# Performance work log

Hardware: AMD Instinct MI355X
Metric: run time of the kernel (lower is better)

Reference implementation:

```python
import jax, jax.numpy as jnp
import numpy as np
import math

B, S, D, H = 2, 2048, 1024, 16
DK = D // H


def setup_inputs() -> dict:
    key = jax.random.key(0)
    ks = jax.random.split(key, 12)
    std = 1.0 / math.sqrt(D)
    inp = {
        "query": jax.random.normal(ks[0], (B, S, D), jnp.float32),
        "key": jax.random.normal(ks[1], (B, S, D), jnp.float32),
        "value": jax.random.normal(ks[2], (B, S, D), jnp.float32),
        # causal mask, broadcast over batch and heads
        "mask": jnp.tril(jnp.ones((S, S), jnp.int32))[None, None, :, :],
        # nn.Linear weights are [out_features, in_features]
        "Wq": jax.random.uniform(ks[3], (D, D), jnp.float32, -std, std),
        "bq": jax.random.uniform(ks[4], (D,), jnp.float32, -std, std),
        "Wk": jax.random.uniform(ks[5], (D, D), jnp.float32, -std, std),
        "bk": jax.random.uniform(ks[6], (D,), jnp.float32, -std, std),
        "Wv": jax.random.uniform(ks[7], (D, D), jnp.float32, -std, std),
        "bv": jax.random.uniform(ks[8], (D,), jnp.float32, -std, std),
        "Wo": jax.random.uniform(ks[9], (D, D), jnp.float32, -std, std),
        "bo": jax.random.uniform(ks[10], (D,), jnp.float32, -std, std),
    }
    return inp


def reference(query, key, value, mask, Wq, bq, Wk, bk, Wv, bv, Wo, bo):
    q = query @ Wq.T + bq  # [B,S,D]
    k = key @ Wk.T + bk
    v = value @ Wv.T + bv
    # Faithful to the original: a raw view (reshape), NOT a head-transpose split.
    q = q.reshape(B, H, S, DK)
    k = k.reshape(B, H, S, DK)
    v = v.reshape(B, H, S, DK)
    scores = jnp.einsum("bhqd,bhkd->bhqk", q, k) / math.sqrt(DK)
    scores = jnp.where(mask == 0, jnp.float32(-1e9), scores)
    weights = jax.nn.softmax(scores, axis=-1)
    # dropout(p=0.1) is identity in eval mode
    context = jnp.einsum("bhqk,bhkd->bhqd", weights, v)
    context = context.transpose(0, 2, 1, 3).reshape(B, S, D)
    return context @ Wo.T + bo
```

## Files before the change

### kernel.cpp

```cpp
#include <hip/hip_runtime.h>
#include <hip/hip_bf16.h>

#define BB 2
#define SS 2048
#define DD 1024
#define HH 16
#define DKK 64

typedef __attribute__((ext_vector_type(4))) float  f32x4;
typedef __attribute__((ext_vector_type(8))) short  s16x8;
typedef __attribute__((ext_vector_type(4))) short  s16x4;
typedef __attribute__((ext_vector_type(4))) float  fvec4;
typedef __attribute__((ext_vector_type(2))) unsigned int u32x2;

__device__ __forceinline__ short f2bs(float f) {
    union { __hip_bfloat16 b; short s; } u;
    u.b = __float2bfloat16(f);
    return u.s;
}

__device__ __forceinline__ unsigned cvtpk(float lo, float hi) {
    unsigned r;
    asm("v_cvt_pk_bf16_f32 %0, %1, %2" : "=v"(r) : "v"(lo), "v"(hi));
    return r;
}

__device__ __forceinline__ void gload_lds16(const short* g, short* l) {
    __builtin_amdgcn_global_load_lds((const __attribute__((address_space(1))) void*)g,
                                     (__attribute__((address_space(3))) void*)l, 16, 0, 0);
}

__global__ __launch_bounds__(256) void cvt_all(
    const float* __restrict__ q,  const float* __restrict__ k,  const float* __restrict__ v,
    const float* __restrict__ wq, const float* __restrict__ wk, const float* __restrict__ wv,
    const float* __restrict__ wo,
    short* __restrict__ qo,  short* __restrict__ ko,  short* __restrict__ vo,
    short* __restrict__ wqo, short* __restrict__ wko, short* __restrict__ wvo,
    short* __restrict__ woo)
{
    const float* src; short* dst; int n;
    switch (blockIdx.y) {
        case 0: src = q;  dst = qo;  n = BB * SS * DD; break;
        case 1: src = k;  dst = ko;  n = BB * SS * DD; break;
        case 2: src = v;  dst = vo;  n = BB * SS * DD; break;
        case 3: src = wq; dst = wqo; n = DD * DD; break;
        case 4: src = wk; dst = wko; n = DD * DD; break;
        case 5: src = wv; dst = wvo; n = DD * DD; break;
        default: src = wo; dst = woo; n = DD * DD; break;
    }
    int i = (blockIdx.x * 256 + threadIdx.x) * 8;
    const int stride = gridDim.x * 256 * 8;
    for (; i < n; i += stride) {
        fvec4 a = *(const fvec4*)&src[i];
        fvec4 b = *(const fvec4*)&src[i + 4];
        s16x8 o;
        o[0] = f2bs(a[0]); o[1] = f2bs(a[1]); o[2] = f2bs(a[2]); o[3] = f2bs(a[3]);
        o[4] = f2bs(b[0]); o[5] = f2bs(b[1]); o[6] = f2bs(b[2]); o[7] = f2bs(b[3]);
        *(s16x8*)&dst[i] = o;
    }
}

template<int BN, int NXSH, bool OUTF32>
__global__ __launch_bounds__(256) void gemm_nt_v2(
    const short* __restrict__ A0, const short* __restrict__ A1, const short* __restrict__ A2,
    const short* __restrict__ B0, const short* __restrict__ B1, const short* __restrict__ B2,
    const float* __restrict__ c0, const float* __restrict__ c1, const float* __restrict__ c2,
    void* __restrict__ O0, void* __restrict__ O1, void* __restrict__ O2,
    float os0, float os1, float os2,
    int ppx, int NY, int KL, int N, int K)
{
    const int d   = blockIdx.x;
    const int xcd = d & 7;
    const int s   = d >> 3;
    const int x   = s & ((1 << NXSH) - 1);
    const int pl  = s >> NXSH;
    const int panel = xcd * ppx + pl;
    const int y   = panel % NY;
    const int z   = panel / NY;

    const short* A    = z == 0 ? A0 : (z == 1 ? A1 : A2);
    const short* Bw   = z == 0 ? B0 : (z == 1 ? B1 : B2);
    const float* bias = z == 0 ? c0 : (z == 1 ? c1 : c2);
    void* Cp          = z == 0 ? O0 : (z == 1 ? O1 : O2);
    const float oscale = z == 0 ? os0 : (z == 1 ? os1 : os2);

    __shared__ short As[128][64];
    __shared__ short Bs[BN][64];

    const int tid  = threadIdx.x;
    const int lane = tid & 63;
    const int wid  = tid >> 6;
    const int r16  = lane & 15;
    const int g    = lane >> 4;
    const int m0   = y * 128;
    const int n0   = x * BN;
    constexpr int MR = 4;
    constexpr int NR = BN / 32;
    const int wr   = (wid >> 1) * 64;
    const int wc   = (wid & 1) * (BN / 2);
    const int srow8 = lane >> 3;
    const int c8    = lane & 7;

    f32x4 acc[MR][NR];
#pragma unroll
    for (int mi = 0; mi < MR; ++mi)
#pragma unroll
        for (int ni = 0; ni < NR; ++ni) acc[mi][ni] = (f32x4){0.f, 0.f, 0.f, 0.f};

    const int csrc = (c8 ^ srow8) * 8;
    const int nk = KL >> 6;
#pragma unroll 1
    for (int kt = 0; kt < nk; ++kt) {
        const int k0 = kt * 64;
        if (kt) __syncthreads();
#pragma unroll
        for (int q = 0; q < 4; ++q) {
            const int r = wid * 32 + q * 8 + srow8;
            gload_lds16(&A[(size_t)(m0 + r) * K + k0 + csrc], &As[wid * 32 + q * 8][0]);
        }
#pragma unroll
        for (int q = 0; q < BN / 32; ++q) {
            const int r = wid * (BN / 4) + q * 8 + srow8;
            gload_lds16(&Bw[(size_t)(n0 + r) * K + k0 + csrc], &Bs[wid * (BN / 4) + q * 8][0]);
        }
        __syncthreads();

#pragma unroll
        for (int kk = 0; kk < 2; ++kk) {
            s16x8 af[MR], bf[NR];
#pragma unroll
            for (int mi = 0; mi < MR; ++mi) {
                const int row = wr + mi * 16 + r16;
                af[mi] = *(const s16x8*)&As[row][((kk * 4 + g) ^ (row & 7)) * 8];
            }
#pragma unroll
            for (int ni = 0; ni < NR; ++ni) {
                const int row = wc + ni * 16 + r16;
                bf[ni] = *(const s16x8*)&Bs[row][((kk * 4 + g) ^ (row & 7)) * 8];
            }
#pragma unroll
            for (int mi = 0; mi < MR; ++mi)
#pragma unroll
                for (int ni = 0; ni < NR; ++ni)
                    acc[mi][ni] = __builtin_amdgcn_mfma_f32_16x16x32_bf16(
                        bf[ni], af[mi], acc[mi][ni], 0, 0, 0);
        }
    }

#pragma unroll
    for (int mi = 0; mi < MR; ++mi) {
        const size_t row = (size_t)(m0 + wr + mi * 16 + r16);
#pragma unroll
        for (int ni = 0; ni < NR; ++ni) {
            const int colb = n0 + wc + ni * 16 + g * 4;
            fvec4 bv;
            if (bias) bv = *(const fvec4*)&bias[colb];
            else      bv = (fvec4){0.f, 0.f, 0.f, 0.f};
            const f32x4 a = acc[mi][ni];
            const float v0 = (a[0] + bv[0]) * oscale;
            const float v1 = (a[1] + bv[1]) * oscale;
            const float v2 = (a[2] + bv[2]) * oscale;
            const float v3 = (a[3] + bv[3]) * oscale;
            if constexpr (OUTF32) {
                fvec4 o; o[0] = v0; o[1] = v1; o[2] = v2; o[3] = v3;
                *(fvec4*)&((float*)Cp)[row * N + colb] = o;
            } else {
                u32x2 w;
                w[0] = cvtpk(v0, v1);
                w[1] = cvtpk(v2, v3);
                *(u32x2*)&((short*)Cp)[row * N + colb] = w;
            }
        }
    }
}

__global__ __launch_bounds__(256) void mha_transpose_v(
    const short* __restrict__ vp, short* __restrict__ vT)
{
    const int st = blockIdx.x;
    const int bh = blockIdx.y;
    const short* src = vp + (size_t)bh * SS * DKK;
    short*       dst = vT + (size_t)bh * SS * DKK;
    const int tid = threadIdx.x;
#pragma unroll
    for (int i = 0; i < 2; ++i) {
        const int c  = tid + i * 256;
        const int dk = c >> 3;
        const int sc = c & 7;
        const int s0 = st * 64 + sc * 8;
        s16x8 v;
#pragma unroll
        for (int j = 0; j < 8; ++j) v[j] = src[(size_t)(s0 + j) * DKK + dk];
        *(s16x8*)&dst[(size_t)dk * SS + s0] = v;
    }
}

__global__ __launch_bounds__(256, 2) void mha_attn(
    const short* __restrict__ qp, const short* __restrict__ kp,
    const short* __restrict__ vT, short* __restrict__ ctx)
{
    __shared__ short Ks[64][64];
    __shared__ short Vs[64][64];
    __shared__ short P[4][16][72];

    const int tid  = threadIdx.x;
    const int wid  = tid >> 6;
    const int lane = tid & 63;
    const int r16  = lane & 15;
    const int g    = lane >> 4;

    const int lin = blockIdx.x;
    const int xcd = lin & 7;
    const int s8  = lin >> 3;
    const int bh  = (xcd << 2) | (s8 & 3);
    const int v   = s8 >> 2;
    const int grp = (v < 16) ? v : (47 - v);
    const int b   = bh >> 4;
    const int h   = bh & 15;

    const short* Qh = qp + (size_t)bh * SS * DKK;
    const short* Kh = kp + (size_t)bh * SS * DKK;
    const short* Vh = vT + (size_t)bh * SS * DKK;

    const int srow = lane >> 3;
    const int csw  = (((lane & 7) ^ srow) & 7) * 8;
    const int r0   = wid * 16;

    const int qr0 = grp * 64 + wid * 16;
    const int nkt = grp + 1;

    const s16x8 qf0 = *(const s16x8*)&Qh[(size_t)(qr0 + r16) * DKK + g * 8];
    const s16x8 qf1 = *(const s16x8*)&Qh[(size_t)(qr0 + r16) * DKK + 32 + g * 8];

    f32x4 po[4];
#pragma unroll
    for (int i = 0; i < 4; ++i) po[i] = (f32x4){0.f, 0.f, 0.f, 0.f};
    float lsum = 0.f;

#pragma unroll 1
    for (int j = 0; j < nkt; ++j) {
        const int k0 = j * 64;
        __syncthreads();
        {
            const int rowA = r0 + srow;
            const int rowB = rowA + 8;
            gload_lds16(&Kh[(size_t)(k0 + rowA) * DKK + csw], &Ks[r0][0]);
            gload_lds16(&Kh[(size_t)(k0 + rowB) * DKK + csw], &Ks[r0 + 8][0]);
            gload_lds16(&Vh[(size_t)rowA * SS + k0 + csw], &Vs[r0][0]);
            gload_lds16(&Vh[(size_t)rowB * SS + k0 + csw], &Vs[r0 + 8][0]);
        }
        __syncthreads();

        f32x4 sc[4];
        __builtin_amdgcn_s_setprio(1);
#pragma unroll
        for (int cg = 0; cg < 4; ++cg) {
            const int R  = cg * 16 + r16;
            const int sw = R & 7;
            const s16x8 kf0 = *(const s16x8*)&Ks[R][((g ^ sw) & 7) * 8];
            const s16x8 kf1 = *(const s16x8*)&Ks[R][(((4 + g) ^ sw) & 7) * 8];
            f32x4 tt = (f32x4){0.f, 0.f, 0.f, 0.f};
            tt = __builtin_amdgcn_mfma_f32_16x16x32_bf16(kf0, qf0, tt, 0, 0, 0);
            tt = __builtin_amdgcn_mfma_f32_16x16x32_bf16(kf1, qf1, tt, 0, 0, 0);
            sc[cg] = tt;
        }
        __builtin_amdgcn_s_setprio(0);

        if (j == nkt - 1) {
#pragma unroll
            for (int cg = 0; cg < 4; ++cg)
#pragma unroll
                for (int r = 0; r < 4; ++r)
                    if (k0 + cg * 16 + g * 4 + r > qr0 + r16) sc[cg][r] = -1e9f;
        }
#pragma unroll
        for (int cg = 0; cg < 4; ++cg) {
            const float p0 = __expf(sc[cg][0]);
            const float p1 = __expf(sc[cg][1]);
            const float p2 = __expf(sc[cg][2]);
            const float p3 = __expf(sc[cg][3]);
            lsum += (p0 + p1) + (p2 + p3);
            u32x2 w;
            w[0] = cvtpk(p0, p1);
            w[1] = cvtpk(p2, p3);
            *(u32x2*)&P[wid][r16][cg * 16 + g * 4] = w;
        }
        const s16x8 pf0 = *(const s16x8*)&P[wid][r16][g * 8];
        const s16x8 pf1 = *(const s16x8*)&P[wid][r16][32 + g * 8];

        __builtin_amdgcn_s_setprio(1);
#pragma unroll
        for (int dg = 0; dg < 4; ++dg) {
            const int Rv = dg * 16 + r16;
            const int sw = Rv & 7;
            const s16x8 vf0 = *(const s16x8*)&Vs[Rv][((g ^ sw) & 7) * 8];
            const s16x8 vf1 = *(const s16x8*)&Vs[Rv][(((4 + g) ^ sw) & 7) * 8];
            po[dg] = __builtin_amdgcn_mfma_f32_16x16x32_bf16(pf0, vf0, po[dg], 0, 0, 0);
            po[dg] = __builtin_amdgcn_mfma_f32_16x16x32_bf16(pf1, vf1, po[dg], 0, 0, 0);
        }
        __builtin_amdgcn_s_setprio(0);
    }

    lsum += __shfl_xor(lsum, 16);
    lsum += __shfl_xor(lsum, 32);
    const float linv = __builtin_amdgcn_rcpf(lsum);
    float rowinv[4];
#pragma unroll
    for (int r = 0; r < 4; ++r)
        rowinv[r] = __shfl(linv, g * 4 + r);
#pragma unroll
    for (int dg = 0; dg < 4; ++dg)
#pragma unroll
        for (int r = 0; r < 4; ++r) {
            const int srw = qr0 + g * 4 + r;
            const float vv = po[dg][r] * rowinv[r];
            ctx[((size_t)(b * SS + srw)) * DD + h * 64 + dg * 16 + r16] = f2bs(vv);
        }
}

extern "C" void kernel_launch(void* const* d_in, const int* in_sizes, int n_in,
                              void* d_out, int out_size, void* d_ws, size_t ws_size,
                              hipStream_t stream) {
    const float* query = (const float*)d_in[0];
    const float* key   = (const float*)d_in[1];
    const float* value = (const float*)d_in[2];
    const float* Wq = (const float*)d_in[4];
    const float* bq = (const float*)d_in[5];
    const float* Wk = (const float*)d_in[6];
    const float* bk = (const float*)d_in[7];
    const float* Wv = (const float*)d_in[8];
    const float* bv = (const float*)d_in[9];
    const float* Wo = (const float*)d_in[10];
    const float* bo = (const float*)d_in[11];
    float* out = (float*)d_out;

    const size_t elems = (size_t)BB * SS * DD;
    const size_t wel   = (size_t)DD * DD;
    short* qx  = (short*)d_ws;
    short* kx  = qx + elems;
    short* vx  = kx + elems;
    short* wqx = vx + elems;
    short* wkx = wqx + wel;
    short* wvx = wkx + wel;
    short* wox = wvx + wel;
    short* qp  = wox + wel;
    short* kp  = qp + elems;
    short* vp  = kp + elems;
    short* vT  = qx;
    short* ctx = vx;

    cvt_all<<<dim3(1024, 7), 256, 0, stream>>>(query, key, value, Wq, Wk, Wv, Wo,
                                               qx, kx, vx, wqx, wkx, wvx, wox);
    gemm_nt_v2<128, 3, false><<<dim3(768), 256, 0, stream>>>(
        qx, kx, vx, wqx, wkx, wvx, bq, bk, bv, qp, kp, vp,
        0.125f, 1.0f, 1.0f, 12, 32, 1024, DD, DD);
    mha_transpose_v<<<dim3(SS / 64, BB * HH), 256, 0, stream>>>(vp, vT);
    mha_attn<<<dim3(1024), 256, 0, stream>>>(qp, kp, vT, ctx);
    gemm_nt_v2<64, 4, true><<<dim3(512), 256, 0, stream>>>(
        ctx, ctx, ctx, wox, wox, wox, bo, bo, bo, out, out, out,
        1.0f, 1.0f, 1.0f, 4, 32, 1024, DD, DD);
}
```

Baseline: 121.1 us.

## Use two waves per attention block, each handling 32 query rows

```diff
diff --git a/kernel.cpp b/kernel.cpp
--- a/kernel.cpp
+++ b/kernel.cpp
@@ -195,13 +195,13 @@
     }
 }
 
-__global__ __launch_bounds__(256, 2) void mha_attn(
+__global__ __launch_bounds__(128) void mha_attn(
     const short* __restrict__ qp, const short* __restrict__ kp,
     const short* __restrict__ vT, short* __restrict__ ctx)
 {
     __shared__ short Ks[64][64];
     __shared__ short Vs[64][64];
-    __shared__ short P[4][16][72];
+    __shared__ short P[2][32][72];
 
     const int tid  = threadIdx.x;
     const int wid  = tid >> 6;
@@ -224,34 +224,40 @@
 
     const int srow = lane >> 3;
     const int csw  = (((lane & 7) ^ srow) & 7) * 8;
-    const int r0   = wid * 16;
-
-    const int qr0 = grp * 64 + wid * 16;
+
+    const int qr0 = grp * 64 + wid * 32;
     const int nkt = grp + 1;
 
-    const s16x8 qf0 = *(const s16x8*)&Qh[(size_t)(qr0 + r16) * DKK + g * 8];
-    const s16x8 qf1 = *(const s16x8*)&Qh[(size_t)(qr0 + r16) * DKK + 32 + g * 8];
-
-    f32x4 po[4];
-#pragma unroll
-    for (int i = 0; i < 4; ++i) po[i] = (f32x4){0.f, 0.f, 0.f, 0.f};
-    float lsum = 0.f;
+    s16x8 qf[2][2];
+#pragma unroll
+    for (int hh = 0; hh < 2; ++hh)
+#pragma unroll
+        for (int sl = 0; sl < 2; ++sl)
+            qf[hh][sl] = *(const s16x8*)&Qh[(size_t)(qr0 + hh * 16 + r16) * DKK + sl * 32 + g * 8];
+
+    f32x4 po[2][4];
+#pragma unroll
+    for (int hh = 0; hh < 2; ++hh)
+#pragma unroll
+        for (int i = 0; i < 4; ++i) po[hh][i] = (f32x4){0.f, 0.f, 0.f, 0.f};
+    float lsum0 = 0.f, lsum1 = 0.f;
 
 #pragma unroll 1
     for (int j = 0; j < nkt; ++j) {
         const int k0 = j * 64;
         __syncthreads();
-        {
-            const int rowA = r0 + srow;
-            const int rowB = rowA + 8;
-            gload_lds16(&Kh[(size_t)(k0 + rowA) * DKK + csw], &Ks[r0][0]);
-            gload_lds16(&Kh[(size_t)(k0 + rowB) * DKK + csw], &Ks[r0 + 8][0]);
-            gload_lds16(&Vh[(size_t)rowA * SS + k0 + csw], &Vs[r0][0]);
-            gload_lds16(&Vh[(size_t)rowB * SS + k0 + csw], &Vs[r0 + 8][0]);
+        if (wid == 0) {
+#pragma unroll
+            for (int q = 0; q < 8; ++q)
+                gload_lds16(&Kh[(size_t)(k0 + q * 8 + srow) * DKK + csw], &Ks[q * 8][0]);
+        } else {
+#pragma unroll
+            for (int q = 0; q < 8; ++q)
+                gload_lds16(&Vh[(size_t)(q * 8 + srow) * SS + k0 + csw], &Vs[q * 8][0]);
         }
         __syncthreads();
 
-        f32x4 sc[4];
+        f32x4 sc[2][4];
         __builtin_amdgcn_s_setprio(1);
 #pragma unroll
         for (int cg = 0; cg < 4; ++cg) {
@@ -259,34 +265,48 @@
             const int sw = R & 7;
             const s16x8 kf0 = *(const s16x8*)&Ks[R][((g ^ sw) & 7) * 8];
             const s16x8 kf1 = *(const s16x8*)&Ks[R][(((4 + g) ^ sw) & 7) * 8];
-            f32x4 tt = (f32x4){0.f, 0.f, 0.f, 0.f};
-            tt = __builtin_amdgcn_mfma_f32_16x16x32_bf16(kf0, qf0, tt, 0, 0, 0);
-            tt = __builtin_amdgcn_mfma_f32_16x16x32_bf16(kf1, qf1, tt, 0, 0, 0);
-            sc[cg] = tt;
+#pragma unroll
+            for (int hh = 0; hh < 2; ++hh) {
+                f32x4 tt = (f32x4){0.f, 0.f, 0.f, 0.f};
+                tt = __builtin_amdgcn_mfma_f32_16x16x32_bf16(kf0, qf[hh][0], tt, 0, 0, 0);
+                tt = __builtin_amdgcn_mfma_f32_16x16x32_bf16(kf1, qf[hh][1], tt, 0, 0, 0);
+                sc[hh][cg] = tt;
+            }
         }
         __builtin_amdgcn_s_setprio(0);
 
         if (j == nkt - 1) {
 #pragma unroll
-            for (int cg = 0; cg < 4; ++cg)
-#pragma unroll
-                for (int r = 0; r < 4; ++r)
-                    if (k0 + cg * 16 + g * 4 + r > qr0 + r16) sc[cg][r] = -1e9f;
-        }
-#pragma unroll
-        for (int cg = 0; cg < 4; ++cg) {
-            const float p0 = __expf(sc[cg][0]);
-            const float p1 = __expf(sc[cg][1]);
-            const float p2 = __expf(sc[cg][2]);
-            const float p3 = __expf(sc[cg][3]);
-            lsum += (p0 + p1) + (p2 + p3);
-            u32x2 w;
-            w[0] = cvtpk(p0, p1);
-            w[1] = cvtpk(p2, p3);
-            *(u32x2*)&P[wid][r16][cg * 16 + g * 4] = w;
-        }
-        const s16x8 pf0 = *(const s16x8*)&P[wid][r16][g * 8];
-        const s16x8 pf1 = *(const s16x8*)&P[wid][r16][32 + g * 8];
+            for (int hh = 0; hh < 2; ++hh)
+#pragma unroll
+                for (int cg = 0; cg < 4; ++cg)
+#pragma unroll
+                    for (int r = 0; r < 4; ++r)
+                        if (k0 + cg * 16 + g * 4 + r > qr0 + hh * 16 + r16)
+                            sc[hh][cg][r] = -1e9f;
+        }
+#pragma unroll
+        for (int hh = 0; hh < 2; ++hh) {
+#pragma unroll
+            for (int cg = 0; cg < 4; ++cg) {
+                const float p0 = __expf(sc[hh][cg][0]);
+                const float p1 = __expf(sc[hh][cg][1]);
+                const float p2 = __expf(sc[hh][cg][2]);
+                const float p3 = __expf(sc[hh][cg][3]);
+                if (hh == 0) lsum0 += (p0 + p1) + (p2 + p3);
+                else         lsum1 += (p0 + p1) + (p2 + p3);
+                u32x2 w;
+                w[0] = cvtpk(p0, p1);
+                w[1] = cvtpk(p2, p3);
+                *(u32x2*)&P[wid][hh * 16 + r16][cg * 16 + g * 4] = w;
+            }
+        }
+        s16x8 pf[2][2];
+#pragma unroll
+        for (int hh = 0; hh < 2; ++hh) {
+            pf[hh][0] = *(const s16x8*)&P[wid][hh * 16 + r16][g * 8];
+            pf[hh][1] = *(const s16x8*)&P[wid][hh * 16 + r16][32 + g * 8];
+        }
 
         __builtin_amdgcn_s_setprio(1);
 #pragma unroll
@@ -295,27 +315,37 @@
             const int sw = Rv & 7;
             const s16x8 vf0 = *(const s16x8*)&Vs[Rv][((g ^ sw) & 7) * 8];
             const s16x8 vf1 = *(const s16x8*)&Vs[Rv][(((4 + g) ^ sw) & 7) * 8];
-            po[dg] = __builtin_amdgcn_mfma_f32_16x16x32_bf16(pf0, vf0, po[dg], 0, 0, 0);
-            po[dg] = __builtin_amdgcn_mfma_f32_16x16x32_bf16(pf1, vf1, po[dg], 0, 0, 0);
+#pragma unroll
+            for (int hh = 0; hh < 2; ++hh) {
+                po[hh][dg] = __builtin_amdgcn_mfma_f32_16x16x32_bf16(pf[hh][0], vf0, po[hh][dg], 0, 0, 0);
+                po[hh][dg] = __builtin_amdgcn_mfma_f32_16x16x32_bf16(pf[hh][1], vf1, po[hh][dg], 0, 0, 0);
+            }
         }
         __builtin_amdgcn_s_setprio(0);
     }
 
-    lsum += __shfl_xor(lsum, 16);
-    lsum += __shfl_xor(lsum, 32);
-    const float linv = __builtin_amdgcn_rcpf(lsum);
-    float rowinv[4];
-#pragma unroll
-    for (int r = 0; r < 4; ++r)
-        rowinv[r] = __shfl(linv, g * 4 + r);
-#pragma unroll
-    for (int dg = 0; dg < 4; ++dg)
-#pragma unroll
-        for (int r = 0; r < 4; ++r) {
-            const int srw = qr0 + g * 4 + r;
-            const float vv = po[dg][r] * rowinv[r];
-            ctx[((size_t)(b * SS + srw)) * DD + h * 64 + dg * 16 + r16] = f2bs(vv);
-        }
+    lsum0 += __shfl_xor(lsum0, 16);
+    lsum0 += __shfl_xor(lsum0, 32);
+    lsum1 += __shfl_xor(lsum1, 16);
+    lsum1 += __shfl_xor(lsum1, 32);
+    const float linv0 = __builtin_amdgcn_rcpf(lsum0);
+    const float linv1 = __builtin_amdgcn_rcpf(lsum1);
+    float rowinv[2][4];
+#pragma unroll
+    for (int r = 0; r < 4; ++r) {
+        rowinv[0][r] = __shfl(linv0, g * 4 + r);
+        rowinv[1][r] = __shfl(linv1, g * 4 + r);
+    }
+#pragma unroll
+    for (int hh = 0; hh < 2; ++hh)
+#pragma unroll
+        for (int dg = 0; dg < 4; ++dg)
+#pragma unroll
+            for (int r = 0; r < 4; ++r) {
+                const int srw = qr0 + hh * 16 + g * 4 + r;
+                const float vv = po[hh][dg][r] * rowinv[hh][r];
+                ctx[((size_t)(b * SS + srw)) * DD + h * 64 + dg * 16 + r16] = f2bs(vv);
+            }
 }
 
 extern "C" void kernel_launch(void* const* d_in, const int* in_sizes, int n_in,
@@ -355,7 +385,7 @@
         qx, kx, vx, wqx, wkx, wvx, bq, bk, bv, qp, kp, vp,
         0.125f, 1.0f, 1.0f, 12, 32, 1024, DD, DD);
     mha_transpose_v<<<dim3(SS / 64, BB * HH), 256, 0, stream>>>(vp, vT);
-    mha_attn<<<dim3(1024), 256, 0, stream>>>(qp, kp, vT, ctx);
+    mha_attn<<<dim3(1024), 128, 0, stream>>>(qp, kp, vT, ctx);
     gemm_nt_v2<64, 4, true><<<dim3(512), 256, 0, stream>>>(
         ctx, ctx, ctx, wox, wox, wox, bo, bo, bo, out, out, out,
         1.0f, 1.0f, 1.0f, 4, 32, 1024, DD, DD);
```

Measured after the change: 131.2 us. 8.4% more time.
